# Optimization experiments

Measured on AMD Instinct MI355X. Metric: run time of the kernel, lower is better.

Reference implementation:

```python
import jax, jax.numpy as jnp
import numpy as np

B, H, W, C = 16, 128, 128, 64


def setup_inputs() -> dict:
    key = jax.random.key(0)
    k1, k2, k3 = jax.random.split(key, 3)
    x = jax.random.normal(k1, (B, H, W, C), dtype=jnp.float32)
    Hout, Wout = 2 * H, 2 * W
    # Argmax-style indices: each pooled element maps into its 2x2 output window.
    dy = jax.random.randint(k2, (B, H, W, C), 0, 2)
    dx = jax.random.randint(k3, (B, H, W, C), 0, 2)
    rows = 2 * jnp.arange(H)[None, :, None, None] + dy      # [B,H,W,C]
    cols = 2 * jnp.arange(W)[None, None, :, None] + dx
    cc = jnp.arange(C)[None, None, None, :]
    indices = ((rows * Wout + cols) * C + cc).astype(jnp.int32)
    return {"x": x, "indices": indices}


def reference(x, indices):
    Bv, Hv, Wv, Cv = x.shape
    Hout, Wout = 2 * Hv, 2 * Wv
    idx = indices.astype(jnp.int32).reshape(-1)
    # Unravel flattened per-batch-element argmax indices (row-major HWC).
    row = idx // (Wout * Cv)                       # x_indices in original
    col = (idx % (Wout * Cv)) // Cv                # y_indices in original
    b = jnp.repeat(jnp.arange(Bv, dtype=jnp.int32), Hv * Wv * Cv)   # t1
    c = jnp.tile(jnp.arange(Cv, dtype=jnp.int32), Bv * Hv * Wv)     # t2
    flat = ((b * Hout + row) * Wout + col) * Cv + c
    # sparse_add on zeros == scatter-add of input values
    out = jnp.zeros((Bv * Hout * Wout * Cv,), x.dtype).at[flat].add(x.reshape(-1))
    return out.reshape(Bv, Hout, Wout, Cv)
```

## Files before the change

kernel.cpp:

```cpp
#include <hip/hip_runtime.h>


typedef float f32x4 __attribute__((ext_vector_type(4)));
typedef int   i32x4 __attribute__((ext_vector_type(4)));

__global__ __launch_bounds__(256) void unpool_window_kernel(
    const f32x4* __restrict__ x,
    const i32x4* __restrict__ ind,
    f32x4*       __restrict__ out,
    int nvec)
{
    int t = blockIdx.x * blockDim.x + threadIdx.x;
    if (t >= nvec) return;

    f32x4 v  = __builtin_nontemporal_load(&x[t]);
    i32x4 id = __builtin_nontemporal_load(&ind[t]);

    int e = t << 2;
    int c = e & 63;
    int w = (e >> 6)  & 127;
    int h = (e >> 13) & 127;
    int b =  e >> 20;

    int pos00 = (h << 15) | (w << 7) | c;
    size_t base = ((size_t)b << 22) + (size_t)pos00;

    int p00 = pos00;
    int p01 = pos00 + 64;
    int p10 = pos00 + 16384;
    int p11 = pos00 + 16448;

    i32x4 cc = {p00 + 0, p00 + 1, p00 + 2, p00 + 3};

    f32x4 s00, s01, s10, s11;
    s00.x = (id.x == cc.x) ? v.x : 0.0f;
    s00.y = (id.y == cc.y) ? v.y : 0.0f;
    s00.z = (id.z == cc.z) ? v.z : 0.0f;
    s00.w = (id.w == cc.w) ? v.w : 0.0f;

    s01.x = (id.x == cc.x + 64) ? v.x : 0.0f;
    s01.y = (id.y == cc.y + 64) ? v.y : 0.0f;
    s01.z = (id.z == cc.z + 64) ? v.z : 0.0f;
    s01.w = (id.w == cc.w + 64) ? v.w : 0.0f;

    s10.x = (id.x == cc.x + 16384) ? v.x : 0.0f;
    s10.y = (id.y == cc.y + 16384) ? v.y : 0.0f;
    s10.z = (id.z == cc.z + 16384) ? v.z : 0.0f;
    s10.w = (id.w == cc.w + 16384) ? v.w : 0.0f;

    s11.x = (id.x == cc.x + 16448) ? v.x : 0.0f;
    s11.y = (id.y == cc.y + 16448) ? v.y : 0.0f;
    s11.z = (id.z == cc.z + 16448) ? v.z : 0.0f;
    s11.w = (id.w == cc.w + 16448) ? v.w : 0.0f;

    f32x4* o = out + (base >> 2);
    __builtin_nontemporal_store(s00, &o[0]);
    __builtin_nontemporal_store(s01, &o[16]);
    __builtin_nontemporal_store(s10, &o[4096]);
    __builtin_nontemporal_store(s11, &o[4112]);
}

extern "C" void kernel_launch(void* const* d_in, const int* in_sizes, int n_in,
                              void* d_out, int out_size, void* d_ws, size_t ws_size,
                              hipStream_t stream) {
    const f32x4* x   = (const f32x4*)d_in[0];
    const i32x4* ind = (const i32x4*)d_in[1];
    f32x4*       out = (f32x4*)d_out;

    int n_elems = in_sizes[0];
    int nvec    = n_elems >> 2;
    int block   = 256;
    int grid    = (nvec + block - 1) / block;

    unpool_window_kernel<<<grid, block, 0, stream>>>(x, ind, out, nvec);
}
```

Before: 70.67 us.

## Parallelize unpool over output vectors instead of input vectors

Switches from one thread per input vector writing four 2x2-window outputs to one thread per output vector that gathers its source input and index. Stores become fully contiguous across a wavefront, and each input vector is read four times, relying on cache hits. The input loads are no longer nontemporal so they can stay in cache. The trade is four times as many threads and redundant input loads in exchange for coalesced writes.

```diff
diff --git a/kernel.cpp b/kernel.cpp
--- a/kernel.cpp
+++ b/kernel.cpp
@@ -4,60 +4,34 @@
 typedef float f32x4 __attribute__((ext_vector_type(4)));
 typedef int   i32x4 __attribute__((ext_vector_type(4)));
 
-__global__ __launch_bounds__(256) void unpool_window_kernel(
+__global__ __launch_bounds__(256) void unpool_out_kernel(
     const f32x4* __restrict__ x,
     const i32x4* __restrict__ ind,
     f32x4*       __restrict__ out,
-    int nvec)
+    int novec)
 {
-    int t = blockIdx.x * blockDim.x + threadIdx.x;
-    if (t >= nvec) return;
+    int o = blockIdx.x * blockDim.x + threadIdx.x;
+    if (o >= novec) return;
 
-    f32x4 v  = __builtin_nontemporal_load(&x[t]);
-    i32x4 id = __builtin_nontemporal_load(&ind[t]);
+    int c4 = o & 15;
+    int wo = (o >> 4)  & 255;
+    int ho = (o >> 12) & 255;
+    int b  =  o >> 20;
 
-    int e = t << 2;
-    int c = e & 63;
-    int w = (e >> 6)  & 127;
-    int h = (e >> 13) & 127;
-    int b =  e >> 20;
+    int in_vec = (b << 18) | ((ho >> 1) << 11) | ((wo >> 1) << 4) | c4;
 
-    int pos00 = (h << 15) | (w << 7) | c;
-    size_t base = ((size_t)b << 22) + (size_t)pos00;
+    f32x4 v  = x[in_vec];
+    i32x4 id = ind[in_vec];
 
-    int p00 = pos00;
-    int p01 = pos00 + 64;
-    int p10 = pos00 + 16384;
-    int p11 = pos00 + 16448;
+    int pos = (ho << 14) | (wo << 6) | (c4 << 2);
 
-    i32x4 cc = {p00 + 0, p00 + 1, p00 + 2, p00 + 3};
+    f32x4 s;
+    s.x = (id.x == pos + 0) ? v.x : 0.0f;
+    s.y = (id.y == pos + 1) ? v.y : 0.0f;
+    s.z = (id.z == pos + 2) ? v.z : 0.0f;
+    s.w = (id.w == pos + 3) ? v.w : 0.0f;
 
-    f32x4 s00, s01, s10, s11;
-    s00.x = (id.x == cc.x) ? v.x : 0.0f;
-    s00.y = (id.y == cc.y) ? v.y : 0.0f;
-    s00.z = (id.z == cc.z) ? v.z : 0.0f;
-    s00.w = (id.w == cc.w) ? v.w : 0.0f;
-
-    s01.x = (id.x == cc.x + 64) ? v.x : 0.0f;
-    s01.y = (id.y == cc.y + 64) ? v.y : 0.0f;
-    s01.z = (id.z == cc.z + 64) ? v.z : 0.0f;
-    s01.w = (id.w == cc.w + 64) ? v.w : 0.0f;
-
-    s10.x = (id.x == cc.x + 16384) ? v.x : 0.0f;
-    s10.y = (id.y == cc.y + 16384) ? v.y : 0.0f;
-    s10.z = (id.z == cc.z + 16384) ? v.z : 0.0f;
-    s10.w = (id.w == cc.w + 16384) ? v.w : 0.0f;
-
-    s11.x = (id.x == cc.x + 16448) ? v.x : 0.0f;
-    s11.y = (id.y == cc.y + 16448) ? v.y : 0.0f;
-    s11.z = (id.z == cc.z + 16448) ? v.z : 0.0f;
-    s11.w = (id.w == cc.w + 16448) ? v.w : 0.0f;
-
-    f32x4* o = out + (base >> 2);
-    __builtin_nontemporal_store(s00, &o[0]);
-    __builtin_nontemporal_store(s01, &o[16]);
-    __builtin_nontemporal_store(s10, &o[4096]);
-    __builtin_nontemporal_store(s11, &o[4112]);
+    __builtin_nontemporal_store(s, &out[o]);
 }
 
 extern "C" void kernel_launch(void* const* d_in, const int* in_sizes, int n_in,
@@ -67,10 +41,9 @@
     const i32x4* ind = (const i32x4*)d_in[1];
     f32x4*       out = (f32x4*)d_out;
 
-    int n_elems = in_sizes[0];
-    int nvec    = n_elems >> 2;
-    int block   = 256;
-    int grid    = (nvec + block - 1) / block;
+    int novec = out_size >> 2;
+    int block = 256;
+    int grid  = (novec + block - 1) / block;
 
-    unpool_window_kernel<<<grid, block, 0, stream>>>(x, ind, out, nvec);
+    unpool_out_kernel<<<grid, block, 0, stream>>>(x, ind, out, novec);
 }
```

Result: faster. 64.20 us (-9.2%).
